# Kernel tuning notes

Hardware: AMD Instinct MI355X
Metric: run time of the kernel (lower is better)

Reference implementation:

```python
import jax, jax.numpy as jnp
import numpy as np

N, D, K, NCB = 65536, 256, 1024, 4


def setup_inputs() -> dict:
    key = jax.random.key(0)
    kz, kc = jax.random.split(key)
    z = jax.random.normal(kz, (N, D), dtype=jnp.float32)
    # nn.Embedding weights init: uniform(-1/k, 1/k)
    codebooks = jax.random.uniform(kc, (NCB, K, D), dtype=jnp.float32,
                                   minval=-1.0 / K, maxval=1.0 / K)
    return {"z": z, "codebooks": codebooks}


def _vq_step(r, W):
    """One VQ codebook pass. r: [N, D], W: [k, D].
    Squared L2 distance via matmul trick: ||r||^2 - 2 r.W^T + ||W||^2,
    same math as sum((r[:,None,:]-W)**2, -1) without the [N,k,D] blowup."""
    r2 = jnp.sum(r * r, axis=-1, keepdims=True)            # [N, 1]
    w2 = jnp.sum(W * W, axis=-1)                           # [k]
    dist = r2 - 2.0 * (r @ W.T) + w2                       # [N, k]
    ind = jnp.argmin(dist, axis=-1)                        # [N]
    z_q = W[ind]                                           # [N, D]
    sg = jax.lax.stop_gradient
    vq_loss = jnp.mean((z_q - sg(r)) ** 2)
    commitment_loss = jnp.mean((r - sg(z_q)) ** 2)
    z_q_st = r + sg(z_q - r)                               # straight-through
    return z_q_st, ind, vq_loss + commitment_loss


def reference(z, codebooks):
    residual = z
    quant_sum = jnp.zeros_like(z)
    inds = []
    total_loss = jnp.zeros((), dtype=z.dtype)
    for i in range(codebooks.shape[0]):  # small fixed loop over codebooks
        z_q, ind, loss = _vq_step(residual, codebooks[i])
        residual = residual - z_q
        quant_sum = quant_sum + z_q
        inds.append(ind)
        total_loss = total_loss + loss
    return quant_sum, jnp.stack(inds, axis=1), total_loss
```

## Files before the change

### kernel.cpp

```cpp
#include <hip/hip_runtime.h>


#define N_TOK 65536
#define DIM   256
#define KCB   1024
#define NCBK  4

#define TM  32
#define TK  256
#define DC  32
#define RST 260
#define WST 34

#define QS_F   ((size_t)N_TOK * DIM)
#define IDX_F  QS_F
#define IDXE_F (IDX_F + (size_t)N_TOK * NCBK)
#define LOSS_F IDXE_F

#define WS_PART_OFF 16384
#define WS_FLAG_OFF 32768

typedef unsigned short u16;
typedef unsigned int   u32;

__device__ __forceinline__ float bf2f(u32 h) { return __uint_as_float(h << 16); }

__device__ __forceinline__ float getv(const void* base, int f32in, size_t elt) {
    if (f32in) return ((const float*)base)[elt];
    return bf2f(((const u16*)base)[elt]);
}

__device__ __forceinline__ void load8(const void* base, int f32in, size_t elt,
                                      float* f) {
    if (f32in) {
        const float* p = (const float*)base + elt;
        #pragma unroll
        for (int e = 0; e < 8; ++e) f[e] = p[e];
    } else {
        uint4 q = *(const uint4*)((const u16*)base + elt);
        f[0] = bf2f(q.x & 0xffffu); f[1] = bf2f(q.x >> 16);
        f[2] = bf2f(q.y & 0xffffu); f[3] = bf2f(q.y >> 16);
        f[4] = bf2f(q.z & 0xffffu); f[5] = bf2f(q.z >> 16);
        f[6] = bf2f(q.w & 0xffffu); f[7] = bf2f(q.w >> 16);
    }
}

__global__ void canary_kernel(float* out) {
    int gid = blockIdx.x * 256 + threadIdx.x;
    size_t pos = IDX_F + (size_t)gid;
    if (pos < IDXE_F) out[pos] = 512.0f;
    if (gid == 0) out[LOSS_F] = 512.0f;
}

__global__ void detect_kernel(const u16* z16, const u16* cb16, int* flags) {
    __shared__ int s0[256], s1[256];
    int tid = threadIdx.x;
    u32 a = z16[tid],  ea = (a >> 7) & 0xffu;
    u32 b = cb16[tid], eb = (b >> 7) & 0xffu;
    s0[tid] = ((ea >= 90u && ea <= 140u) || ((a & 0x7fffu) == 0u)) ? 1 : 0;
    s1[tid] = ((eb >= 90u && eb <= 140u) || ((b & 0x7fffu) == 0u)) ? 1 : 0;
    __syncthreads();
    for (int st = 128; st > 0; st >>= 1) {
        if (tid < st) { s0[tid] += s0[tid + st]; s1[tid] += s1[tid + st]; }
        __syncthreads();
    }
    if (tid == 0) { flags[0] = (s0[0] < 218) ? 1 : 0;
                    flags[1] = (s1[0] < 218) ? 1 : 0; }
}

__device__ __forceinline__ float np128_sq_g(const void* base, int f32in, size_t off) {
    float S[16];
    #pragma unroll
    for (int l = 0; l < 16; ++l) {
        float A[8];
        #pragma unroll
        for (int j = 0; j < 8; ++j) {
            float x = getv(base, f32in, off + 16 * j + l);
            A[j] = x * x;
        }
        S[l] = ((A[0] + A[1]) + (A[2] + A[3])) + ((A[4] + A[5]) + (A[6] + A[7]));
    }
    float B1[8], B2[4];
    #pragma unroll
    for (int l = 0; l < 8; ++l) B1[l] = S[l] + S[l + 8];
    #pragma unroll
    for (int l = 0; l < 4; ++l) B2[l] = B1[l] + B1[l + 4];
    return (B2[0] + B2[2]) + (B2[1] + B2[3]);
}

__device__ __forceinline__ float np128_sq_lds(const float* a) {
    float S[16];
    #pragma unroll
    for (int l = 0; l < 16; ++l) {
        float A[8];
        #pragma unroll
        for (int j = 0; j < 8; ++j) { float x = a[16 * j + l]; A[j] = x * x; }
        S[l] = ((A[0] + A[1]) + (A[2] + A[3])) + ((A[4] + A[5]) + (A[6] + A[7]));
    }
    float B1[8], B2[4];
    #pragma unroll
    for (int l = 0; l < 8; ++l) B1[l] = S[l] + S[l + 8];
    #pragma unroll
    for (int l = 0; l < 4; ++l) B2[l] = B1[l] + B1[l + 4];
    return (B2[0] + B2[2]) + (B2[1] + B2[3]);
}

__global__ void w2_kernel(const void* cbs, float* w2f, const int* flags) {
    int kf = blockIdx.x * 256 + threadIdx.x;
    const int fc = flags[1];
    size_t base = (size_t)kf * DIM;
    w2f[kf] = np128_sq_g(cbs, fc, base) + np128_sq_g(cbs, fc, base + 128);
}

__global__ __launch_bounds__(256, 2)
void rq_kernel(const void* z, const void* cbs, const float* w2f,
               float* out, double* partials, const int* flags) {
    __shared__ float  Rld[TM * RST];
    __shared__ float  Wld[TK * WST];
    __shared__ float  candv[TM * 33];
    __shared__ int    candi[TM * 33];
    __shared__ float  r2s[TM];
    __shared__ int    bestk[TM];
    __shared__ double dred[256];

    const int fz = flags[0], fc = flags[1];
    const int tid  = threadIdx.x;
    const int tx   = tid & 31;
    const int ty   = tid >> 5;
    const int row0 = blockIdx.x * TM;

    float q[32];
    #pragma unroll
    for (int e = 0; e < 32; ++e) q[e] = 0.f;

    for (int it = 0; it < 4; ++it) {
        int flat = it * 256 + tid;
        int r = flat >> 5, c8 = flat & 31;
        float f[8];
        load8(z, fz, (size_t)(row0 + r) * DIM + c8 * 8, f);
        int base = r * RST + c8 * 8;
        #pragma unroll
        for (int e = 0; e < 8; ++e) Rld[base + e] = f[e];
    }
    double lsum = 0.0;

    for (int cb = 0; cb < NCBK; ++cb) {
        const size_t cbW = (size_t)cb * KCB * DIM;
        const float* w2c = w2f + cb * KCB;

        __syncthreads();
        if (tid < TM) {
            const float* a = &Rld[tid * RST];
            r2s[tid] = np128_sq_lds(a) + np128_sq_lds(a + 128);
        }
        __syncthreads();

        float r2v[4];
        #pragma unroll
        for (int i = 0; i < 4; ++i) r2v[i] = r2s[ty + 8 * i];

        float bval[4]; int bidx[4];
        #pragma unroll
        for (int i = 0; i < 4; ++i) { bval[i] = __uint_as_float(0x7f7fffffu); bidx[i] = 0; }

        for (int kt = 0; kt < KCB / TK; ++kt) {
            float acc[4][8];
            #pragma unroll
            for (int i = 0; i < 4; ++i)
                #pragma unroll
                for (int j = 0; j < 8; ++j) acc[i][j] = 0.f;

            for (int dc = 0; dc < DIM / DC; ++dc) {
                __syncthreads();
                #pragma unroll
                for (int it = 0; it < 4; ++it) {
                    int k = it * 64 + (tid >> 2);
                    int dp = (tid & 3) * 8;
                    float f[8];
                    load8(cbs, fc, cbW + (size_t)(kt * TK + k) * DIM + dc * DC + dp, f);
                    int base = k * WST + dp;
                    #pragma unroll
                    for (int e = 0; e < 8; ++e) Wld[base + e] = f[e];
                }
                __syncthreads();

                #pragma unroll
                for (int dd = 0; dd < DC / 4; ++dd) {
                    float av[4][4];
                    #pragma unroll
                    for (int i = 0; i < 4; ++i) {
                        int ab = (ty + 8 * i) * RST + dc * DC + dd * 4;
                        #pragma unroll
                        for (int e = 0; e < 4; ++e) av[i][e] = Rld[ab + e];
                    }
                    float bv[8][4];
                    #pragma unroll
                    for (int j = 0; j < 8; ++j) {
                        int bb = (tx + 32 * j) * WST + dd * 4;
                        #pragma unroll
                        for (int e = 0; e < 4; ++e) bv[j][e] = Wld[bb + e];
                    }
                    #pragma unroll
                    for (int i = 0; i < 4; ++i)
                        #pragma unroll
                        for (int j = 0; j < 8; ++j) {
                            float s = acc[i][j];
                            s = fmaf(av[i][0], bv[j][0], s);
                            s = fmaf(av[i][1], bv[j][1], s);
                            s = fmaf(av[i][2], bv[j][2], s);
                            s = fmaf(av[i][3], bv[j][3], s);
                            acc[i][j] = s;
                        }
                }
            }
            #pragma unroll
            for (int j = 0; j < 8; ++j) {
                int k = kt * TK + tx + 32 * j;
                float w2k = w2c[k];
                #pragma unroll
                for (int i = 0; i < 4; ++i) {
                    float t2   = r2v[i] - 2.0f * acc[i][j];
                    float dist = t2 + w2k;
                    if (dist < bval[i] || (dist == bval[i] && k < bidx[i])) {
                        bval[i] = dist; bidx[i] = k;
                    }
                }
            }
        }
        __syncthreads();
        #pragma unroll
        for (int i = 0; i < 4; ++i) {
            int r = ty + 8 * i;
            candv[r * 33 + tx] = bval[i];
            candi[r * 33 + tx] = bidx[i];
        }
        __syncthreads();
        if (tid < TM) {
            float best = candv[tid * 33];
            int   bi   = candi[tid * 33];
            for (int t = 1; t < 32; ++t) {
                float v = candv[tid * 33 + t];
                int  ix = candi[tid * 33 + t];
                if (v < best || (v == best && ix < bi)) { best = v; bi = ix; }
            }
            bestk[tid] = bi;
            size_t pos = IDX_F + (size_t)(row0 + tid) * NCBK + cb;
            if (pos < IDXE_F) out[pos] = (float)bi;
        }
        __syncthreads();
        #pragma unroll
        for (int it = 0; it < 4; ++it) {
            int flat = it * 256 + tid;
            int r = flat >> 5, c8 = flat & 31;
            int kb = bestk[r];
            float f[8];
            load8(cbs, fc, cbW + (size_t)kb * DIM + c8 * 8, f);
            int base = r * RST + c8 * 8;
            #pragma unroll
            for (int e = 0; e < 8; ++e) {
                float rv = Rld[base + e];
                float t  = f[e] - rv;
                float s  = rv + t;
                float rn = rv - s;
                Rld[base + e] = rn;
                q[it * 8 + e] = q[it * 8 + e] + s;
                lsum += (double)t * (double)t;
            }
        }
        __syncthreads();
    }

    #pragma unroll
    for (int it = 0; it < 4; ++it) {
        int flat = it * 256 + tid;
        int r = flat >> 5, c8 = flat & 31;
        size_t pos = (size_t)(row0 + r) * DIM + c8 * 8;
        if (pos + 8 <= QS_F) {
            #pragma unroll
            for (int e = 0; e < 8; ++e) out[pos + e] = q[it * 8 + e];
        }
    }

    dred[tid] = lsum;
    __syncthreads();
    for (int s = 128; s > 0; s >>= 1) {
        if (tid < s) dred[tid] += dred[tid + s];
        __syncthreads();
    }
    if (tid == 0) partials[blockIdx.x] = dred[0];
}

__global__ void loss_final(const double* partials, float* out) {
    __shared__ double sred[256];
    int tid = threadIdx.x;
    double s = 0.0;
    for (int q = 0; q < 8; ++q) s += partials[tid + 256 * q];
    sred[tid] = s;
    __syncthreads();
    for (int st = 128; st > 0; st >>= 1) {
        if (tid < st) sred[tid] += sred[tid + st];
        __syncthreads();
    }
    if (tid == 0)
        out[LOSS_F] = (float)(2.0 * sred[0] / 16777216.0);
}

extern "C" void kernel_launch(void* const* d_in, const int* in_sizes, int n_in,
                              void* d_out, int out_size, void* d_ws, size_t ws_size,
                              hipStream_t stream) {
    (void)n_in; (void)out_size; (void)ws_size;
    const void* z;
    const void* cbs;
    if (in_sizes[0] == 16777216) { z = d_in[0]; cbs = d_in[1]; }
    else                         { z = d_in[1]; cbs = d_in[0]; }

    float*  out      = (float*)d_out;
    float*  w2f      = (float*)d_ws;
    double* partials = (double*)((char*)d_ws + WS_PART_OFF);
    int*    flags    = (int*)((char*)d_ws + WS_FLAG_OFF);

    canary_kernel<<<1024, 256, 0, stream>>>(out);
    detect_kernel<<<1, 256, 0, stream>>>((const u16*)z, (const u16*)cbs, flags);
    w2_kernel<<<16, 256, 0, stream>>>(cbs, w2f, flags);
    rq_kernel<<<N_TOK / TM, 256, 0, stream>>>(z, cbs, w2f, out, partials, flags);
    loss_final<<<1, 256, 0, stream>>>(partials, out);
}
```

Before: 2.633 ms.

## Retile distance GEMM to 8x8 register microtile with wider codebook tile

Each thread now computes an 8-row by 8-codeword accumulator tile instead of 4x8. The codebook tile widens to 512 codewords with a 16-wide depth chunk and a new stride. Shared-memory loads become float4/float2 vectors, global fp32 loads use float4, and the candidate buffers alias the W tile to save LDS. The goal is more FMAs per LDS read and fewer tile passes over K, at the cost of higher register pressure under launch_bounds(256,2), a 64-way final argmin scan, and more barriers per depth step.

```diff
diff --git a/kernel.cpp b/kernel.cpp
--- a/kernel.cpp
+++ b/kernel.cpp
@@ -7,10 +7,10 @@
 #define NCBK  4
 
 #define TM  32
-#define TK  256
-#define DC  32
+#define TK  512
+#define DC  16
 #define RST 260
-#define WST 34
+#define WST 18
 
 #define QS_F   ((size_t)N_TOK * DIM)
 #define IDX_F  QS_F
@@ -33,9 +33,10 @@
 __device__ __forceinline__ void load8(const void* base, int f32in, size_t elt,
                                       float* f) {
     if (f32in) {
-        const float* p = (const float*)base + elt;
-        #pragma unroll
-        for (int e = 0; e < 8; ++e) f[e] = p[e];
+        const float4* p = (const float4*)((const float*)base + elt);
+        float4 a = p[0], b = p[1];
+        f[0] = a.x; f[1] = a.y; f[2] = a.z; f[3] = a.w;
+        f[4] = b.x; f[5] = b.y; f[6] = b.z; f[7] = b.w;
     } else {
         uint4 q = *(const uint4*)((const u16*)base + elt);
         f[0] = bf2f(q.x & 0xffffu); f[1] = bf2f(q.x >> 16);
@@ -117,16 +118,19 @@
                float* out, double* partials, const int* flags) {
     __shared__ float  Rld[TM * RST];
     __shared__ float  Wld[TK * WST];
-    __shared__ float  candv[TM * 33];
-    __shared__ int    candi[TM * 33];
     __shared__ float  r2s[TM];
     __shared__ int    bestk[TM];
     __shared__ double dred[256];
+
+    float* candv = Wld;
+    int*   candi = (int*)(Wld + TM * 65);
 
     const int fz = flags[0], fc = flags[1];
     const int tid  = threadIdx.x;
     const int tx   = tid & 31;
     const int ty   = tid >> 5;
+    const int rowg = ty & 3;
+    const int cg   = ty >> 2;
     const int row0 = blockIdx.x * TM;
 
     float q[32];
@@ -155,18 +159,18 @@
         }
         __syncthreads();
 
-        float r2v[4];
-        #pragma unroll
-        for (int i = 0; i < 4; ++i) r2v[i] = r2s[ty + 8 * i];
-
-        float bval[4]; int bidx[4];
-        #pragma unroll
-        for (int i = 0; i < 4; ++i) { bval[i] = __uint_as_float(0x7f7fffffu); bidx[i] = 0; }
+        float r2v[8];
+        #pragma unroll
+        for (int i = 0; i < 8; ++i) r2v[i] = r2s[rowg + 4 * i];
+
+        float bval[8]; int bidx[8];
+        #pragma unroll
+        for (int i = 0; i < 8; ++i) { bval[i] = __uint_as_float(0x7f7fffffu); bidx[i] = 0; }
 
         for (int kt = 0; kt < KCB / TK; ++kt) {
-            float acc[4][8];
+            float acc[8][8];
             #pragma unroll
-            for (int i = 0; i < 4; ++i)
+            for (int i = 0; i < 8; ++i)
                 #pragma unroll
                 for (int j = 0; j < 8; ++j) acc[i][j] = 0.f;
 
@@ -174,51 +178,53 @@
                 __syncthreads();
                 #pragma unroll
                 for (int it = 0; it < 4; ++it) {
-                    int k = it * 64 + (tid >> 2);
-                    int dp = (tid & 3) * 8;
+                    int flat = it * 256 + tid;
+                    int k  = flat >> 1;
+                    int dp = (flat & 1) * 8;
                     float f[8];
                     load8(cbs, fc, cbW + (size_t)(kt * TK + k) * DIM + dc * DC + dp, f);
-                    int base = k * WST + dp;
-                    #pragma unroll
-                    for (int e = 0; e < 8; ++e) Wld[base + e] = f[e];
+                    int wb = k * WST + dp;
+                    *(float2*)&Wld[wb]     = make_float2(f[0], f[1]);
+                    *(float2*)&Wld[wb + 2] = make_float2(f[2], f[3]);
+                    *(float2*)&Wld[wb + 4] = make_float2(f[4], f[5]);
+                    *(float2*)&Wld[wb + 6] = make_float2(f[6], f[7]);
                 }
                 __syncthreads();
 
                 #pragma unroll
                 for (int dd = 0; dd < DC / 4; ++dd) {
-                    float av[4][4];
+                    float av[8][4];
                     #pragma unroll
-                    for (int i = 0; i < 4; ++i) {
-                        int ab = (ty + 8 * i) * RST + dc * DC + dd * 4;
-                        #pragma unroll
-                        for (int e = 0; e < 4; ++e) av[i][e] = Rld[ab + e];
+                    for (int i = 0; i < 8; ++i) {
+                        const float4 va = *(const float4*)
+                            &Rld[(rowg + 4 * i) * RST + dc * DC + dd * 4];
+                        av[i][0] = va.x; av[i][1] = va.y;
+                        av[i][2] = va.z; av[i][3] = va.w;
                     }
-                    float bv[8][4];
                     #pragma unroll
                     for (int j = 0; j < 8; ++j) {
-                        int bb = (tx + 32 * j) * WST + dd * 4;
+                        const int c = tx + 32 * j + 256 * cg;
+                        const float2* wp = (const float2*)&Wld[c * WST + dd * 4];
+                        const float2 b01 = wp[0];
+                        const float2 b23 = wp[1];
                         #pragma unroll
-                        for (int e = 0; e < 4; ++e) bv[j][e] = Wld[bb + e];
-                    }
-                    #pragma unroll
-                    for (int i = 0; i < 4; ++i)
-                        #pragma unroll
-                        for (int j = 0; j < 8; ++j) {
+                        for (int i = 0; i < 8; ++i) {
                             float s = acc[i][j];
-                            s = fmaf(av[i][0], bv[j][0], s);
-                            s = fmaf(av[i][1], bv[j][1], s);
-                            s = fmaf(av[i][2], bv[j][2], s);
-                            s = fmaf(av[i][3], bv[j][3], s);
+                            s = fmaf(av[i][0], b01.x, s);
+                            s = fmaf(av[i][1], b01.y, s);
+                            s = fmaf(av[i][2], b23.x, s);
+                            s = fmaf(av[i][3], b23.y, s);
                             acc[i][j] = s;
                         }
+                    }
                 }
             }
             #pragma unroll
             for (int j = 0; j < 8; ++j) {
-                int k = kt * TK + tx + 32 * j;
-                float w2k = w2c[k];
+                const int k = kt * TK + tx + 32 * j + 256 * cg;
+                const float w2k = w2c[k];
                 #pragma unroll
-                for (int i = 0; i < 4; ++i) {
+                for (int i = 0; i < 8; ++i) {
                     float t2   = r2v[i] - 2.0f * acc[i][j];
                     float dist = t2 + w2k;
                     if (dist < bval[i] || (dist == bval[i] && k < bidx[i])) {
@@ -229,18 +235,18 @@
         }
         __syncthreads();
         #pragma unroll
-        for (int i = 0; i < 4; ++i) {
-            int r = ty + 8 * i;
-            candv[r * 33 + tx] = bval[i];
-            candi[r * 33 + tx] = bidx[i];
+        for (int i = 0; i < 8; ++i) {
+            int r = rowg + 4 * i;
+            candv[r * 65 + tx + 32 * cg] = bval[i];
+            candi[r * 65 + tx + 32 * cg] = bidx[i];
         }
         __syncthreads();
         if (tid < TM) {
-            float best = candv[tid * 33];
-            int   bi   = candi[tid * 33];
-            for (int t = 1; t < 32; ++t) {
-                float v = candv[tid * 33 + t];
-                int  ix = candi[tid * 33 + t];
+            float best = candv[tid * 65];
+            int   bi   = candi[tid * 65];
+            for (int t = 1; t < 64; ++t) {
+                float v = candv[tid * 65 + t];
+                int  ix = candi[tid * 65 + t];
                 if (v < best || (v == best && ix < bi)) { best = v; bi = ix; }
             }
             bestk[tid] = bi;
```

Result: slower. 2.806 ms (+6.6%).
